# Optimization experiments

Hardware: AMD Instinct MI355X
Metric: run time of the kernel (lower is better)

Reference implementation:

```python
import jax, jax.numpy as jnp
import numpy as np

A_BITS = 4          # a_bits
W_BITS = 4          # w_bits / w_slices (w_slices = 1)
NUM_CHUNKS = 9      # ceil(in_ch*9 / 64) = ceil(576/64)
BN_EPS = 1e-5


def quantize_weight(w, bits):
    # WeightQuantize STE: uniform symmetric quantization, straight-through on clipped range
    n = 2.0 ** (bits - 1) - 1.0
    c = jnp.clip(w, -1.0, 1.0)
    q = jnp.round(c * n) / n
    return c + jax.lax.stop_gradient(q - c)


def create_input_stream(a, a_bits):
    # residual multi-bit binarization into a_bits sign planes, x ~= sum_i plane_i / 2^(i+1)
    x = jnp.clip(a, -1.0, 1.0)
    planes = []
    r = x
    for i in range(a_bits):
        s = jnp.where(r >= 0, 1.0, -1.0)
        planes.append(x + jax.lax.stop_gradient(s - x))  # STE plane
        r = r - s / (2.0 ** (i + 1))
    return jnp.stack(planes, 0)  # [a_bits, B, C*9, L]


def unfold3x3(x, pad=1):
    # torch F.unfold(kernel=3, stride=1) ordering: (C, kh, kw) flattened channel-major
    B, C, H, W = x.shape
    xp = jnp.pad(x, ((0, 0), (0, 0), (pad, pad), (pad, pad)))
    cols = jnp.stack([xp[:, :, i:i + H, j:j + W] for i in range(3) for j in range(3)], axis=2)
    return cols.reshape(B, C * 9, H * W)  # [B, C*9, L]


def mtj(x, gamma, beta, key):
    mean = x.mean(axis=(0, 2), keepdims=True)
    var = x.var(axis=(0, 2), keepdims=True)  # biased, as torch BN
    normed = (x - mean) / jnp.sqrt(var + BN_EPS) * gamma[None, :, None] + beta[None, :, None]
    t = jnp.tanh(4.0 * normed)
    rand = jax.random.uniform(key, x.shape, minval=-1.0, maxval=1.0)
    out = jnp.where(t > rand, 1.0, -1.0)
    out = jnp.where(normed == 0.0, 0.0, out)
    c = jnp.clip(normed, -1.0, 1.0)
    return c + jax.lax.stop_gradient(out - c)


def setup_inputs() -> dict:
    key = jax.random.key(0)
    k1, k2 = jax.random.split(key)
    inputs = jax.random.normal(k1, (8, 64, 32, 32), dtype=jnp.float32)
    weight = jax.random.normal(k2, (128, 64, 3, 3), dtype=jnp.float32) * (2.0 / (64 * 9)) ** 0.5
    gamma = jnp.ones((128,), jnp.float32)
    beta = jnp.zeros((128,), jnp.float32)
    return {"inputs": inputs, "weight": weight, "gamma": gamma, "beta": beta}


def reference(inputs, weight, gamma, beta):
    O = weight.shape[0]
    # weight standardization (per output filter; std is unbiased as torch .std())
    wf = weight.reshape(O, -1)
    bw = weight - wf.mean(-1)[:, None, None, None]
    std = bw.reshape(O, -1).std(-1, ddof=1)
    bw = bw / std[:, None, None, None]
    qw = quantize_weight(bw, W_BITS)                      # [O, C, 3, 3]
    a = unfold3x3(inputs)                                 # [B, C*9, L]
    stream = create_input_stream(a, A_BITS)               # [A, B, C*9, L]
    A, B, CK, L = stream.shape
    cs = CK // NUM_CHUNKS
    x = stream.reshape(A * B, NUM_CHUNKS, cs, L)          # chunked along the C*9 axis
    fw = qw.reshape(O, NUM_CHUNKS, cs)                    # flattened weight chunks
    # per-chunk F.linear, vectorized over chunks: [nc, A*B, O, L]
    lt = jnp.einsum('ngkl,ogk->gnol', x, fw)
    keys = jax.random.split(jax.random.key(42), NUM_CHUNKS)
    pre = jax.vmap(lambda t, k: mtj(t, gamma, beta, k))(lt, keys) / NUM_CHUNKS
    out = pre.sum(0)                                      # sum chunks (w_slices=1 -> identity combine)
    # gen_image_vector_and_sum: recombine activation bit-planes
    out = out.reshape(A, B, O, L)
    wts = (2.0 ** -(jnp.arange(A, dtype=jnp.float32) + 1.0)).reshape(A, 1, 1, 1)
    out = (out * wts).sum(0)
    HW = int(np.sqrt(L))
    return out.reshape(B, O, HW, HW)                      # F.fold with (1,1) kernel
```

## Files before the change

### kernel.cpp

```cpp
#include <hip/hip_runtime.h>
#include <stdint.h>

#ifndef PRNG_PARTITIONABLE
#define PRNG_PARTITIONABLE 1
#endif

#define ONE_M_U 0.99999994039535522461f

__device__ __forceinline__ void tf_4a(uint32_t& x0, uint32_t& x1){
  x0 += x1; x1 = (x1<<13)|(x1>>19); x1 ^= x0;
  x0 += x1; x1 = (x1<<15)|(x1>>17); x1 ^= x0;
  x0 += x1; x1 = (x1<<26)|(x1>>6);  x1 ^= x0;
  x0 += x1; x1 = (x1<<6) |(x1>>26); x1 ^= x0;
}
__device__ __forceinline__ void tf_4b(uint32_t& x0, uint32_t& x1){
  x0 += x1; x1 = (x1<<17)|(x1>>15); x1 ^= x0;
  x0 += x1; x1 = (x1<<29)|(x1>>3);  x1 ^= x0;
  x0 += x1; x1 = (x1<<16)|(x1>>16); x1 ^= x0;
  x0 += x1; x1 = (x1<<24)|(x1>>8);  x1 ^= x0;
}
__device__ __forceinline__ void threefry2x32(uint32_t k0, uint32_t k1, uint32_t& x0, uint32_t& x1){
  uint32_t k2 = k0 ^ k1 ^ 0x1BD11BDAu;
  x0 += k0; x1 += k1;
  tf_4a(x0,x1); x0 += k1; x1 += k2 + 1u;
  tf_4b(x0,x1); x0 += k2; x1 += k0 + 2u;
  tf_4a(x0,x1); x0 += k0; x1 += k1 + 3u;
  tf_4b(x0,x1); x0 += k1; x1 += k2 + 4u;
  tf_4a(x0,x1); x0 += k2; x1 += k0 + 5u;
}

__device__ __forceinline__ float bits_to_unit(uint32_t b){
  #pragma clang fp contract(off)
  float f = __uint_as_float((b >> 9) | 0x3f800000u) - 1.0f;
  float r = f * 2.0f + (-1.0f);
  return __builtin_fmaxf(-1.0f, r);
}

__device__ __forceinline__ float xla_tanh_f32(float x){
  #pragma clang fp contract(off)
  float ax = __builtin_fabsf(x);
  float xc = __builtin_fminf(__builtin_fmaxf(x, -9.0f), 9.0f);
  float x2 = xc * xc;
  float nm = -2.76076847742355e-16f;
  nm = x2 * nm + 2.00018790482477e-13f;
  nm = x2 * nm + -8.60467152213735e-11f;
  nm = x2 * nm + 5.12229709037114e-08f;
  nm = x2 * nm + 1.48572235717979e-05f;
  nm = x2 * nm + 6.37261928875436e-04f;
  nm = x2 * nm + 4.89352455891786e-03f;
  nm = xc * nm;
  float dn = 1.19825839466702e-06f;
  dn = x2 * dn + 1.18534705686654e-04f;
  dn = x2 * dn + 2.26843463243900e-03f;
  dn = x2 * dn + 4.89352518554385e-03f;
  float res = nm / dn;
  return (ax < 0.0004f) ? x : res;
}

__device__ __forceinline__ float dot64(unsigned long long sw, unsigned long long dw,
                                       const float* w){
  float acc = 0.0f;
  #pragma unroll
  for (int k = 0; k < 64; ++k){
    float mag = ((dw >> k) & 1ull) ? ONE_M_U : 1.0f;
    float p   = ((sw >> k) & 1ull) ? mag : -mag;
    acc = __builtin_fmaf(p, w[k], acc);
  }
  return acc;
}

#define QW_OFF   0u
#define QWT_OFF  294912u
#define SGN_OFF  589824u
#define DIM_OFF  2949120u
#define KEYS_OFF 5308416u
#define MV_OFF   5308544u
#define LT_OFF   5318656u
#define LT_BYTES 150994944u
#define WS_NEEDED_FAST (LT_OFF + LT_BYTES)

__global__ __launch_bounds__(64) void k_weights(const float* __restrict__ W,
        float* __restrict__ qw, float* __restrict__ qwT, uint32_t* __restrict__ keys){
  #pragma clang fp contract(off)
  __shared__ float  bwL[576];
  __shared__ double red[64];
  int o = blockIdx.x, t = threadIdx.x;
  double s = 0.0;
  for (int j = t; j < 576; j += 64) s += (double)W[o*576 + j];
  red[t] = s; __syncthreads();
  for (int k = 32; k > 0; k >>= 1){ if (t < k) red[t] += red[t+k]; __syncthreads(); }
  float mean1 = (float)(red[0] / 576.0);
  __syncthreads();
  for (int j = t; j < 576; j += 64) bwL[j] = W[o*576 + j] - mean1;
  __syncthreads();
  s = 0.0;
  for (int j = t; j < 576; j += 64) s += (double)bwL[j];
  red[t] = s; __syncthreads();
  for (int k = 32; k > 0; k >>= 1){ if (t < k) red[t] += red[t+k]; __syncthreads(); }
  float mean2 = (float)(red[0] / 576.0);
  __syncthreads();
  s = 0.0;
  for (int j = t; j < 576; j += 64){ float c = bwL[j] - mean2; float sq = c * c; s += (double)sq; }
  red[t] = s; __syncthreads();
  for (int k = 32; k > 0; k >>= 1){ if (t < k) red[t] += red[t+k]; __syncthreads(); }
  float varf = (float)(red[0] / 575.0);
  float stdv = __builtin_sqrtf(varf);
  __syncthreads();
  for (int j = t; j < 576; j += 64){
    float b2 = bwL[j] / stdv;
    float c  = __builtin_fminf(__builtin_fmaxf(b2, -1.0f), 1.0f);
    float q  = __builtin_rintf(c * 7.0f) / 7.0f;
    float fwd = c + (q - c);
    int g = j >> 6, k = j & 63;
    qw [(g*128 + o)*64 + k] = fwd;
    qwT[(g*64  + k)*128 + o] = fwd;
  }
  if (o == 0 && t == 0){
#if PRNG_PARTITIONABLE
    for (int g = 0; g < 9; ++g){
      uint32_t x0 = 0u, x1 = (uint32_t)g;
      threefry2x32(0u, 42u, x0, x1);
      keys[2*g] = x0; keys[2*g+1] = x1;
    }
#else
    uint32_t outv[18];
    for (int i = 0; i < 9; ++i){
      uint32_t x0 = (uint32_t)i, x1 = (uint32_t)(9 + i);
      threefry2x32(0u, 42u, x0, x1);
      outv[i] = x0; outv[9+i] = x1;
    }
    for (int j = 0; j < 18; ++j) keys[j] = outv[j];
#endif
  }
}

__global__ __launch_bounds__(256) void k_stream(const float* __restrict__ X,
        unsigned long long* __restrict__ sgn, unsigned long long* __restrict__ dimw){
  #pragma clang fp contract(off)
  int g = blockIdx.y;
  int tid = blockIdx.x * 256 + threadIdx.x;
  int b = tid >> 10, l = tid & 1023;
  int h = l >> 5, w = l & 31;
  unsigned long long sw0=0ull, sw1=0ull, sw2=0ull, sw3=0ull;
  unsigned long long dw0=0ull, dw1=0ull, dw2=0ull, dw3=0ull;
  const float* Xb = X + b*64*1024;
  int ck0 = g*64;
  #pragma unroll
  for (int i = 0; i < 64; ++i){
    int ck = ck0 + i;
    int c = ck / 9, kp = ck % 9;
    int di = kp / 3 - 1, dj = kp % 3 - 1;
    int hh = h + di, ww = w + dj;
    float v = 0.0f;
    if (hh >= 0 && hh < 32 && ww >= 0 && ww < 32)
      v = Xb[(c*32 + hh)*32 + ww];
    float x = __builtin_fminf(__builtin_fmaxf(v, -1.0f), 1.0f);
    float r = x;
    {
      float sv = (r >= 0.0f) ? 1.0f : -1.0f;
      float d  = sv - x;
      float p  = x + d;
      if (sv > 0.0f) sw0 |= (1ull << i);
      if (__builtin_fabsf(p) < 1.0f) dw0 |= (1ull << i);
      r = r - sv * 0.5f;
    }
    {
      float sv = (r >= 0.0f) ? 1.0f : -1.0f;
      float d  = sv - x;
      float p  = x + d;
      if (sv > 0.0f) sw1 |= (1ull << i);
      if (__builtin_fabsf(p) < 1.0f) dw1 |= (1ull << i);
      r = r - sv * 0.25f;
    }
    {
      float sv = (r >= 0.0f) ? 1.0f : -1.0f;
      float d  = sv - x;
      float p  = x + d;
      if (sv > 0.0f) sw2 |= (1ull << i);
      if (__builtin_fabsf(p) < 1.0f) dw2 |= (1ull << i);
      r = r - sv * 0.125f;
    }
    {
      float sv = (r >= 0.0f) ? 1.0f : -1.0f;
      float d  = sv - x;
      float p  = x + d;
      if (sv > 0.0f) sw3 |= (1ull << i);
      if (__builtin_fabsf(p) < 1.0f) dw3 |= (1ull << i);
      r = r - sv * 0.0625f;
    }
  }
  sgn [((0*8+b)*9 + g)*1024 + l] = sw0;
  sgn [((1*8+b)*9 + g)*1024 + l] = sw1;
  sgn [((2*8+b)*9 + g)*1024 + l] = sw2;
  sgn [((3*8+b)*9 + g)*1024 + l] = sw3;
  dimw[((0*8+b)*9 + g)*1024 + l] = dw0;
  dimw[((1*8+b)*9 + g)*1024 + l] = dw1;
  dimw[((2*8+b)*9 + g)*1024 + l] = dw2;
  dimw[((3*8+b)*9 + g)*1024 + l] = dw3;
}

__global__ __launch_bounds__(256) void k_gemm(const float* __restrict__ qwT,
        const unsigned long long* __restrict__ sgn, const unsigned long long* __restrict__ dimw,
        float* __restrict__ lt){
  __shared__ float wT[64*128];
  __shared__ float pL[64*64];
  int lchunk = blockIdx.x, g = blockIdx.y, n = blockIdx.z;
  int t = threadIdx.x;
  for (int j = t; j < 8192; j += 256) wT[j] = qwT[g*8192 + j];
  {
    int lc = t & 63, kq = t >> 6;
    unsigned long long sw = sgn [(n*9+g)*1024 + lchunk*64 + lc];
    unsigned long long dw = dimw[(n*9+g)*1024 + lchunk*64 + lc];
    #pragma unroll
    for (int kk = 0; kk < 16; ++kk){
      int k = kq*16 + kk;
      float mag = ((dw >> k) & 1ull) ? ONE_M_U : 1.0f;
      float p   = ((sw >> k) & 1ull) ? mag : -mag;
      pL[k*64 + lc] = p;
    }
  }
  __syncthreads();
  int otile = t & 31, ltile = t >> 5;
  const float4* wT4 = (const float4*)wT;
  const float4* pL4 = (const float4*)pL;
  float acc[4][8];
  #pragma unroll
  for (int i = 0; i < 4; ++i)
    #pragma unroll
    for (int j = 0; j < 8; ++j) acc[i][j] = 0.0f;
  #pragma unroll 8
  for (int k = 0; k < 64; ++k){
    float4 wv = wT4[k*32 + otile];
    float4 pa = pL4[k*16 + ltile*2];
    float4 pb = pL4[k*16 + ltile*2 + 1];
    float wr[4] = {wv.x, wv.y, wv.z, wv.w};
    float pr[8] = {pa.x, pa.y, pa.z, pa.w, pb.x, pb.y, pb.z, pb.w};
    #pragma unroll
    for (int i = 0; i < 4; ++i)
      #pragma unroll
      for (int j = 0; j < 8; ++j)
        acc[i][j] = __builtin_fmaf(pr[j], wr[i], acc[i][j]);
  }
  int o0 = otile*4, l0 = lchunk*64 + ltile*8;
  #pragma unroll
  for (int i = 0; i < 4; ++i){
    float* dst = lt + (((n*9+g)*128 + o0 + i) * 1024) + l0;
    float4 s0 = {acc[i][0], acc[i][1], acc[i][2], acc[i][3]};
    float4 s1 = {acc[i][4], acc[i][5], acc[i][6], acc[i][7]};
    ((float4*)dst)[0] = s0;
    ((float4*)dst)[1] = s1;
  }
}

__global__ __launch_bounds__(256) void k_stats_fast(const float* __restrict__ lt,
        float* __restrict__ mv){
  #pragma clang fp contract(off)
  __shared__ double red[256];
  int g = blockIdx.x >> 7, o = blockIdx.x & 127, t = threadIdx.x;
  double s1 = 0.0;
  for (int n = 0; n < 32; ++n){
    const float* p = lt + ((size_t)((n*9+g)*128 + o)) * 1024;
    for (int j = 0; j < 4; ++j) s1 += (double)p[t + j*256];
  }
  red[t] = s1; __syncthreads();
  for (int k = 128; k > 0; k >>= 1){ if (t < k) red[t] += red[t+k]; __syncthreads(); }
  float mean = (float)(red[0] / 32768.0);
  __syncthreads();
  double s2 = 0.0;
  for (int n = 0; n < 32; ++n){
    const float* p = lt + ((size_t)((n*9+g)*128 + o)) * 1024;
    for (int j = 0; j < 4; ++j){
      float tv = p[t + j*256];
      float c = tv - mean;
      float sq = c * c;
      s2 += (double)sq;
    }
  }
  red[t] = s2; __syncthreads();
  for (int k = 128; k > 0; k >>= 1){ if (t < k) red[t] += red[t+k]; __syncthreads(); }
  if (t == 0){
    float var = (float)(red[0] / 32768.0);
    float den = __builtin_sqrtf(var + 1e-5f);
    mv[(g*128+o)*2]   = mean;
    mv[(g*128+o)*2+1] = den;
  }
}

__global__ __launch_bounds__(256) void k_out_fast(const float* __restrict__ lt,
        const float* __restrict__ mv, const uint32_t* __restrict__ keys,
        const float* __restrict__ gamma, const float* __restrict__ beta,
        float* __restrict__ out){
  #pragma clang fp contract(off)
  __shared__ float    mvL[18];
  __shared__ uint32_t kL[18];
  int bi = blockIdx.x;
  int lc = bi & 3, o = (bi >> 2) & 127, b = bi >> 9;
  int t = threadIdx.x;
  if (t < 18){ mvL[t] = mv[((t>>1)*128 + o)*2 + (t&1)]; kL[t] = keys[t]; }
  __syncthreads();
  int l = lc*256 + t;
  float gma = gamma[o], bta = beta[o];
  float S[4] = {0.0f, 0.0f, 0.0f, 0.0f};
  for (int g = 0; g < 9; ++g){
    float rnd[4];
#if PRNG_PARTITIONABLE
    #pragma unroll
    for (int a = 0; a < 4; ++a){
      uint32_t m = (uint32_t)((a*8 + b)*131072 + o*1024 + l);
      uint32_t x0 = 0u, x1 = m;
      threefry2x32(kL[2*g], kL[2*g+1], x0, x1);
      rnd[a] = bits_to_unit(x0 ^ x1);
    }
#else
    #pragma unroll
    for (int a01 = 0; a01 < 2; ++a01){
      uint32_t m = (uint32_t)((a01*8 + b)*131072 + o*1024 + l);
      uint32_t x0 = m, x1 = m + 2097152u;
      threefry2x32(kL[2*g], kL[2*g+1], x0, x1);
      rnd[a01]     = bits_to_unit(x0);
      rnd[a01 + 2] = bits_to_unit(x1);
    }
#endif
    float mean = mvL[2*g], den = mvL[2*g+1];
    #pragma unroll
    for (int a = 0; a < 4; ++a){
      int n = a*8 + b;
      float tv = lt[((size_t)((n*9+g)*128 + o)) * 1024 + l];
      float normed = (tv - mean) / den * gma + bta;
      float th = xla_tanh_f32(4.0f * normed);
      float dec = (th > rnd[a]) ? 1.0f : -1.0f;
      if (normed == 0.0f) dec = 0.0f;
      float cc  = __builtin_fminf(__builtin_fmaxf(normed, -1.0f), 1.0f);
      float fwd = cc + (dec - cc);
      float pre = fwd / 9.0f;
      S[a] = S[a] + pre;
    }
  }
  float z = S[0] * 0.5f;
  z = z + S[1] * 0.25f;
  z = z + S[2] * 0.125f;
  z = z + S[3] * 0.0625f;
  out[(b*128 + o)*1024 + l] = z;
}

__global__ __launch_bounds__(256) void k_stats_slow(const float* __restrict__ qw,
        const unsigned long long* __restrict__ sgn, const unsigned long long* __restrict__ dimw,
        float* __restrict__ mv){
  #pragma clang fp contract(off)
  __shared__ double red[256];
  int g = blockIdx.x >> 7, o = blockIdx.x & 127, t = threadIdx.x;
  float wr[64];
  #pragma unroll
  for (int k = 0; k < 64; ++k) wr[k] = qw[(g*128 + o)*64 + k];
  double s1 = 0.0;
  for (int n = 0; n < 32; ++n){
    const unsigned long long* sp = sgn  + (n*9 + g)*1024;
    const unsigned long long* dp = dimw + (n*9 + g)*1024;
    for (int j = 0; j < 4; ++j){
      int l = t + j*256;
      float tv = dot64(sp[l], dp[l], wr);
      s1 += (double)tv;
    }
  }
  red[t] = s1; __syncthreads();
  for (int k = 128; k > 0; k >>= 1){ if (t < k) red[t] += red[t+k]; __syncthreads(); }
  float mean = (float)(red[0] / 32768.0);
  __syncthreads();
  double s2 = 0.0;
  for (int n = 0; n < 32; ++n){
    const unsigned long long* sp = sgn  + (n*9 + g)*1024;
    const unsigned long long* dp = dimw + (n*9 + g)*1024;
    for (int j = 0; j < 4; ++j){
      int l = t + j*256;
      float tv = dot64(sp[l], dp[l], wr);
      float c = tv - mean;
      float sq = c * c;
      s2 += (double)sq;
    }
  }
  red[t] = s2; __syncthreads();
  for (int k = 128; k > 0; k >>= 1){ if (t < k) red[t] += red[t+k]; __syncthreads(); }
  if (t == 0){
    float var = (float)(red[0] / 32768.0);
    float den = __builtin_sqrtf(var + 1e-5f);
    mv[(g*128+o)*2]   = mean;
    mv[(g*128+o)*2+1] = den;
  }
}

__global__ __launch_bounds__(256) void k_out_slow(const float* __restrict__ qw,
        const unsigned long long* __restrict__ sgn, const unsigned long long* __restrict__ dimw,
        const float* __restrict__ mv, const uint32_t* __restrict__ keys,
        const float* __restrict__ gamma, const float* __restrict__ beta,
        float* __restrict__ out){
  #pragma clang fp contract(off)
  __shared__ float    wv[576];
  __shared__ float    mvL[18];
  __shared__ uint32_t kL[18];
  int bi = blockIdx.x;
  int lc = bi & 3, o = (bi >> 2) & 127, b = bi >> 9;
  int t = threadIdx.x;
  for (int j = t; j < 576; j += 256) wv[j] = qw[((j >> 6)*128 + o)*64 + (j & 63)];
  if (t < 18){ mvL[t] = mv[((t>>1)*128 + o)*2 + (t&1)]; kL[t] = keys[t]; }
  __syncthreads();
  int l = lc*256 + t;
  float gma = gamma[o], bta = beta[o];
  float S[4] = {0.0f, 0.0f, 0.0f, 0.0f};
  for (int g = 0; g < 9; ++g){
    float rnd[4];
#if PRNG_PARTITIONABLE
    #pragma unroll
    for (int a = 0; a < 4; ++a){
      uint32_t m = (uint32_t)((a*8 + b)*131072 + o*1024 + l);
      uint32_t x0 = 0u, x1 = m;
      threefry2x32(kL[2*g], kL[2*g+1], x0, x1);
      rnd[a] = bits_to_unit(x0 ^ x1);
    }
#else
    #pragma unroll
    for (int a01 = 0; a01 < 2; ++a01){
      uint32_t m = (uint32_t)((a01*8 + b)*131072 + o*1024 + l);
      uint32_t x0 = m, x1 = m + 2097152u;
      threefry2x32(kL[2*g], kL[2*g+1], x0, x1);
      rnd[a01]     = bits_to_unit(x0);
      rnd[a01 + 2] = bits_to_unit(x1);
    }
#endif
    float mean = mvL[2*g], den = mvL[2*g+1];
    float wr[64];
    #pragma unroll
    for (int k = 0; k < 64; ++k) wr[k] = wv[g*64 + k];
    #pragma unroll
    for (int a = 0; a < 4; ++a){
      int n = a*8 + b;
      float tv = dot64(sgn[(n*9+g)*1024 + l], dimw[(n*9+g)*1024 + l], wr);
      float normed = (tv - mean) / den * gma + bta;
      float th = xla_tanh_f32(4.0f * normed);
      float dec = (th > rnd[a]) ? 1.0f : -1.0f;
      if (normed == 0.0f) dec = 0.0f;
      float cc  = __builtin_fminf(__builtin_fmaxf(normed, -1.0f), 1.0f);
      float fwd = cc + (dec - cc);
      float pre = fwd / 9.0f;
      S[a] = S[a] + pre;
    }
  }
  float z = S[0] * 0.5f;
  z = z + S[1] * 0.25f;
  z = z + S[2] * 0.125f;
  z = z + S[3] * 0.0625f;
  out[(b*128 + o)*1024 + l] = z;
}

extern "C" void kernel_launch(void* const* d_in, const int* in_sizes, int n_in,
                              void* d_out, int out_size, void* d_ws, size_t ws_size,
                              hipStream_t stream){
  (void)in_sizes; (void)n_in; (void)out_size;
  const float* inp   = (const float*)d_in[0];
  const float* wgt   = (const float*)d_in[1];
  const float* gamma = (const float*)d_in[2];
  const float* beta  = (const float*)d_in[3];
  float* out = (float*)d_out;
  char* ws = (char*)d_ws;
  float*              qw   = (float*)(ws + QW_OFF);
  float*              qwT  = (float*)(ws + QWT_OFF);
  unsigned long long* sgn  = (unsigned long long*)(ws + SGN_OFF);
  unsigned long long* dimw = (unsigned long long*)(ws + DIM_OFF);
  uint32_t*           keys = (uint32_t*)(ws + KEYS_OFF);
  float*              mv   = (float*)(ws + MV_OFF);
  float*              lt   = (float*)(ws + LT_OFF);

  hipLaunchKernelGGL(k_weights, dim3(128),    dim3(64),  0, stream, wgt, qw, qwT, keys);
  hipLaunchKernelGGL(k_stream,  dim3(32, 9),  dim3(256), 0, stream, inp, sgn, dimw);
  if (ws_size >= (size_t)WS_NEEDED_FAST){
    hipLaunchKernelGGL(k_gemm,       dim3(16, 9, 32), dim3(256), 0, stream, qwT, sgn, dimw, lt);
    hipLaunchKernelGGL(k_stats_fast, dim3(1152),      dim3(256), 0, stream, lt, mv);
    hipLaunchKernelGGL(k_out_fast,   dim3(4096),      dim3(256), 0, stream, lt, mv, keys,
                       gamma, beta, out);
  } else {
    hipLaunchKernelGGL(k_stats_slow, dim3(1152), dim3(256), 0, stream, qw, sgn, dimw, mv);
    hipLaunchKernelGGL(k_out_slow,   dim3(4096), dim3(256), 0, stream, qw, sgn, dimw, mv, keys,
                       gamma, beta, out);
  }
}
```

Measured before the change: 331.3 us.

## Fuse per-channel mean partials into GEMM epilogue and retile GEMM to 128x128

The GEMM now computes a 128x128 output tile per block from padded LDS float4 tiles taken straight from qw, which removes the transposed weight copy. Its epilogue reduces per-channel partial sums in double precision and writes them to a new partial buffer. A small k_mean kernel turns those partials into the channel mean, so the stats kernel only makes one pass over lt for the variance. The output kernel loop order is swapped so each bit-plane walks the chunks with a single base pointer. This spends one extra launch and more workspace to avoid re-reading the 150MB lt buffer for the mean.

After: 322.2 us. -2.7%, faster.

```diff
diff --git a/kernel.cpp b/kernel.cpp
--- a/kernel.cpp
+++ b/kernel.cpp
@@ -70,17 +70,18 @@
 }
 
 #define QW_OFF   0u
-#define QWT_OFF  294912u
-#define SGN_OFF  589824u
-#define DIM_OFF  2949120u
-#define KEYS_OFF 5308416u
-#define MV_OFF   5308544u
-#define LT_OFF   5318656u
+#define SGN_OFF  294912u
+#define DIM_OFF  2654208u
+#define KEYS_OFF 5013504u
+#define MV_OFF   5013632u
+#define LT_OFF   5023744u
 #define LT_BYTES 150994944u
-#define WS_NEEDED_FAST (LT_OFF + LT_BYTES)
+#define PART_OFF (LT_OFF + LT_BYTES)
+#define PART_BYTES 2359296u
+#define WS_NEEDED_FAST (PART_OFF + PART_BYTES)
 
 __global__ __launch_bounds__(64) void k_weights(const float* __restrict__ W,
-        float* __restrict__ qw, float* __restrict__ qwT, uint32_t* __restrict__ keys){
+        float* __restrict__ qw, uint32_t* __restrict__ keys){
   #pragma clang fp contract(off)
   __shared__ float  bwL[576];
   __shared__ double red[64];
@@ -113,7 +114,6 @@
     float fwd = c + (q - c);
     int g = j >> 6, k = j & 63;
     qw [(g*128 + o)*64 + k] = fwd;
-    qwT[(g*64  + k)*128 + o] = fwd;
   }
   if (o == 0 && t == 0){
 #if PRNG_PARTITIONABLE
@@ -158,32 +158,28 @@
     float r = x;
     {
       float sv = (r >= 0.0f) ? 1.0f : -1.0f;
-      float d  = sv - x;
-      float p  = x + d;
+      float d  = sv - x; float p = x + d;
       if (sv > 0.0f) sw0 |= (1ull << i);
       if (__builtin_fabsf(p) < 1.0f) dw0 |= (1ull << i);
       r = r - sv * 0.5f;
     }
     {
       float sv = (r >= 0.0f) ? 1.0f : -1.0f;
-      float d  = sv - x;
-      float p  = x + d;
+      float d  = sv - x; float p = x + d;
       if (sv > 0.0f) sw1 |= (1ull << i);
       if (__builtin_fabsf(p) < 1.0f) dw1 |= (1ull << i);
       r = r - sv * 0.25f;
     }
     {
       float sv = (r >= 0.0f) ? 1.0f : -1.0f;
-      float d  = sv - x;
-      float p  = x + d;
+      float d  = sv - x; float p = x + d;
       if (sv > 0.0f) sw2 |= (1ull << i);
       if (__builtin_fabsf(p) < 1.0f) dw2 |= (1ull << i);
       r = r - sv * 0.125f;
     }
     {
       float sv = (r >= 0.0f) ? 1.0f : -1.0f;
-      float d  = sv - x;
-      float p  = x + d;
+      float d  = sv - x; float p = x + d;
       if (sv > 0.0f) sw3 |= (1ull << i);
       if (__builtin_fabsf(p) < 1.0f) dw3 |= (1ull << i);
       r = r - sv * 0.0625f;
@@ -199,73 +195,106 @@
   dimw[((3*8+b)*9 + g)*1024 + l] = dw3;
 }
 
-__global__ __launch_bounds__(256) void k_gemm(const float* __restrict__ qwT,
+__global__ __launch_bounds__(256) void k_gemm(const float* __restrict__ qw,
         const unsigned long long* __restrict__ sgn, const unsigned long long* __restrict__ dimw,
-        float* __restrict__ lt){
-  __shared__ float wT[64*128];
-  __shared__ float pL[64*64];
-  int lchunk = blockIdx.x, g = blockIdx.y, n = blockIdx.z;
+        float* __restrict__ lt, double* __restrict__ part){
+  __shared__ float4 wS[128*17];
+  __shared__ float4 pS[128*17];
+  int lq = blockIdx.x, g = blockIdx.y, n = blockIdx.z;
   int t = threadIdx.x;
-  for (int j = t; j < 8192; j += 256) wT[j] = qwT[g*8192 + j];
   {
-    int lc = t & 63, kq = t >> 6;
-    unsigned long long sw = sgn [(n*9+g)*1024 + lchunk*64 + lc];
-    unsigned long long dw = dimw[(n*9+g)*1024 + lchunk*64 + lc];
-    #pragma unroll
-    for (int kk = 0; kk < 16; ++kk){
-      int k = kq*16 + kk;
-      float mag = ((dw >> k) & 1ull) ? ONE_M_U : 1.0f;
-      float p   = ((sw >> k) & 1ull) ? mag : -mag;
-      pL[k*64 + lc] = p;
-    }
-  }
-  __syncthreads();
-  int otile = t & 31, ltile = t >> 5;
-  const float4* wT4 = (const float4*)wT;
-  const float4* pL4 = (const float4*)pL;
-  float acc[4][8];
-  #pragma unroll
-  for (int i = 0; i < 4; ++i)
+    int o = t >> 4, kq = t & 15;
+    const float4* qw4 = (const float4*)qw;
+    #pragma unroll
+    for (int i = 0; i < 8; ++i){
+      int oo = o + 16*i;
+      wS[oo*17 + kq] = qw4[(g*128 + oo)*16 + kq];
+    }
+  }
+  {
+    int l = t >> 1, kh = t & 1;
+    unsigned long long sw = sgn [(n*9+g)*1024 + lq*128 + l];
+    unsigned long long dw = dimw[(n*9+g)*1024 + lq*128 + l];
+    #pragma unroll
+    for (int kq = 0; kq < 8; ++kq){
+      int kqq = kh*8 + kq;
+      float4 v;
+      {
+        int k = kqq*4;
+        float m0 = ((dw>>k)&1ull)?ONE_M_U:1.0f; v.x = ((sw>>k)&1ull)?m0:-m0;
+        float m1 = ((dw>>(k+1))&1ull)?ONE_M_U:1.0f; v.y = ((sw>>(k+1))&1ull)?m1:-m1;
+        float m2 = ((dw>>(k+2))&1ull)?ONE_M_U:1.0f; v.z = ((sw>>(k+2))&1ull)?m2:-m2;
+        float m3 = ((dw>>(k+3))&1ull)?ONE_M_U:1.0f; v.w = ((sw>>(k+3))&1ull)?m3:-m3;
+      }
+      pS[l*17 + kqq] = v;
+    }
+  }
+  __syncthreads();
+  int ot = t >> 4, ltl = t & 15;
+  float acc[8][8];
+  #pragma unroll
+  for (int i = 0; i < 8; ++i)
     #pragma unroll
     for (int j = 0; j < 8; ++j) acc[i][j] = 0.0f;
-  #pragma unroll 8
-  for (int k = 0; k < 64; ++k){
-    float4 wv = wT4[k*32 + otile];
-    float4 pa = pL4[k*16 + ltile*2];
-    float4 pb = pL4[k*16 + ltile*2 + 1];
-    float wr[4] = {wv.x, wv.y, wv.z, wv.w};
-    float pr[8] = {pa.x, pa.y, pa.z, pa.w, pb.x, pb.y, pb.z, pb.w};
-    #pragma unroll
-    for (int i = 0; i < 4; ++i)
+  for (int kq = 0; kq < 16; ++kq){
+    float wr[8][4], pr[8][4];
+    #pragma unroll
+    for (int i = 0; i < 8; ++i) *(float4*)wr[i] = wS[(ot*8+i)*17 + kq];
+    #pragma unroll
+    for (int j = 0; j < 8; ++j) *(float4*)pr[j] = pS[(ltl+16*j)*17 + kq];
+    #pragma unroll
+    for (int e = 0; e < 4; ++e)
       #pragma unroll
-      for (int j = 0; j < 8; ++j)
-        acc[i][j] = __builtin_fmaf(pr[j], wr[i], acc[i][j]);
-  }
-  int o0 = otile*4, l0 = lchunk*64 + ltile*8;
-  #pragma unroll
-  for (int i = 0; i < 4; ++i){
-    float* dst = lt + (((n*9+g)*128 + o0 + i) * 1024) + l0;
-    float4 s0 = {acc[i][0], acc[i][1], acc[i][2], acc[i][3]};
-    float4 s1 = {acc[i][4], acc[i][5], acc[i][6], acc[i][7]};
-    ((float4*)dst)[0] = s0;
-    ((float4*)dst)[1] = s1;
-  }
-}
-
-__global__ __launch_bounds__(256) void k_stats_fast(const float* __restrict__ lt,
+      for (int i = 0; i < 8; ++i)
+        #pragma unroll
+        for (int j = 0; j < 8; ++j)
+          acc[i][j] = __builtin_fmaf(pr[j][e], wr[i][e], acc[i][j]);
+  }
+  #pragma unroll
+  for (int i = 0; i < 8; ++i){
+    int o = ot*8 + i;
+    float* dst = lt + ((size_t)((n*9+g)*128 + o))*1024 + lq*128 + ltl;
+    #pragma unroll
+    for (int j = 0; j < 8; ++j) dst[16*j] = acc[i][j];
+  }
+  double ps[8];
+  #pragma unroll
+  for (int i = 0; i < 8; ++i){
+    double s = 0.0;
+    #pragma unroll
+    for (int j = 0; j < 8; ++j) s += (double)acc[i][j];
+    ps[i] = s;
+  }
+  __syncthreads();
+  double* red = (double*)pS;
+  #pragma unroll
+  for (int i = 0; i < 8; ++i) red[(ot*8+i)*16 + ltl] = ps[i];
+  __syncthreads();
+  if (t < 128){
+    double s = 0.0;
+    #pragma unroll
+    for (int q = 0; q < 16; ++q) s += red[t*16 + q];
+    part[((size_t)g*128 + t)*256 + n*8 + lq] = s;
+  }
+}
+
+__global__ __launch_bounds__(64) void k_mean(const double* __restrict__ part,
+        float* __restrict__ mv){
+  __shared__ double red[64];
+  int go = blockIdx.x, t = threadIdx.x;
+  double s = 0.0;
+  for (int idx = t; idx < 256; idx += 64) s += part[(size_t)go*256 + idx];
+  red[t] = s; __syncthreads();
+  for (int k = 32; k > 0; k >>= 1){ if (t < k) red[t] += red[t+k]; __syncthreads(); }
+  if (t == 0) mv[go*2] = (float)(red[0] / 32768.0);
+}
+
+__global__ __launch_bounds__(256) void k_stats2(const float* __restrict__ lt,
         float* __restrict__ mv){
   #pragma clang fp contract(off)
   __shared__ double red[256];
   int g = blockIdx.x >> 7, o = blockIdx.x & 127, t = threadIdx.x;
-  double s1 = 0.0;
-  for (int n = 0; n < 32; ++n){
-    const float* p = lt + ((size_t)((n*9+g)*128 + o)) * 1024;
-    for (int j = 0; j < 4; ++j) s1 += (double)p[t + j*256];
-  }
-  red[t] = s1; __syncthreads();
-  for (int k = 128; k > 0; k >>= 1){ if (t < k) red[t] += red[t+k]; __syncthreads(); }
-  float mean = (float)(red[0] / 32768.0);
-  __syncthreads();
+  float mean = mv[(g*128+o)*2];
   double s2 = 0.0;
   for (int n = 0; n < 32; ++n){
     const float* p = lt + ((size_t)((n*9+g)*128 + o)) * 1024;
@@ -281,7 +310,6 @@
   if (t == 0){
     float var = (float)(red[0] / 32768.0);
     float den = __builtin_sqrtf(var + 1e-5f);
-    mv[(g*128+o)*2]   = mean;
     mv[(g*128+o)*2+1] = den;
   }
 }
@@ -300,41 +328,39 @@
   __syncthreads();
   int l = lc*256 + t;
   float gma = gamma[o], bta = beta[o];
-  float S[4] = {0.0f, 0.0f, 0.0f, 0.0f};
-  for (int g = 0; g < 9; ++g){
-    float rnd[4];
+  float S[4];
+  #pragma unroll
+  for (int a = 0; a < 4; ++a){
+    int n = a*8 + b;
 #if PRNG_PARTITIONABLE
-    #pragma unroll
-    for (int a = 0; a < 4; ++a){
-      uint32_t m = (uint32_t)((a*8 + b)*131072 + o*1024 + l);
+    uint32_t m = (uint32_t)(n*131072 + o*1024 + l);
+#endif
+    const float* pa = lt + ((size_t)(n*9)*128 + o)*1024 + l;
+    float Sa = 0.0f;
+    for (int g = 0; g < 9; ++g){
+      float rnd;
+#if PRNG_PARTITIONABLE
       uint32_t x0 = 0u, x1 = m;
       threefry2x32(kL[2*g], kL[2*g+1], x0, x1);
-      rnd[a] = bits_to_unit(x0 ^ x1);
-    }
+      rnd = bits_to_unit(x0 ^ x1);
 #else
-    #pragma unroll
-    for (int a01 = 0; a01 < 2; ++a01){
-      uint32_t m = (uint32_t)((a01*8 + b)*131072 + o*1024 + l);
-      uint32_t x0 = m, x1 = m + 2097152u;
+      uint32_t mm = (uint32_t)(((a&1)*8 + b)*131072 + o*1024 + l);
+      uint32_t x0 = mm, x1 = mm + 2097152u;
       threefry2x32(kL[2*g], kL[2*g+1], x0, x1);
-      rnd[a01]     = bits_to_unit(x0);
-      rnd[a01 + 2] = bits_to_unit(x1);
-    }
+      rnd = (a < 2) ? bits_to_unit(x0) : bits_to_unit(x1);
 #endif
-    float mean = mvL[2*g], den = mvL[2*g+1];
-    #pragma unroll
-    for (int a = 0; a < 4; ++a){
-      int n = a*8 + b;
-      float tv = lt[((size_t)((n*9+g)*128 + o)) * 1024 + l];
+      float mean = mvL[2*g], den = mvL[2*g+1];
+      float tv = pa[g*131072];
       float normed = (tv - mean) / den * gma + bta;
       float th = xla_tanh_f32(4.0f * normed);
-      float dec = (th > rnd[a]) ? 1.0f : -1.0f;
+      float dec = (th > rnd) ? 1.0f : -1.0f;
       if (normed == 0.0f) dec = 0.0f;
       float cc  = __builtin_fminf(__builtin_fmaxf(normed, -1.0f), 1.0f);
       float fwd = cc + (dec - cc);
       float pre = fwd / 9.0f;
-      S[a] = S[a] + pre;
-    }
+      Sa = Sa + pre;
+    }
+    S[a] = Sa;
   }
   float z = S[0] * 0.5f;
   z = z + S[1] * 0.25f;
@@ -462,19 +488,20 @@
   float* out = (float*)d_out;
   char* ws = (char*)d_ws;
   float*              qw   = (float*)(ws + QW_OFF);
-  float*              qwT  = (float*)(ws + QWT_OFF);
   unsigned long long* sgn  = (unsigned long long*)(ws + SGN_OFF);
   unsigned long long* dimw = (unsigned long long*)(ws + DIM_OFF);
   uint32_t*           keys = (uint32_t*)(ws + KEYS_OFF);
   float*              mv   = (float*)(ws + MV_OFF);
   float*              lt   = (float*)(ws + LT_OFF);
-
-  hipLaunchKernelGGL(k_weights, dim3(128),    dim3(64),  0, stream, wgt, qw, qwT, keys);
+  double*             part = (double*)(ws + PART_OFF);
+
+  hipLaunchKernelGGL(k_weights, dim3(128),    dim3(64),  0, stream, wgt, qw, keys);
   hipLaunchKernelGGL(k_stream,  dim3(32, 9),  dim3(256), 0, stream, inp, sgn, dimw);
   if (ws_size >= (size_t)WS_NEEDED_FAST){
-    hipLaunchKernelGGL(k_gemm,       dim3(16, 9, 32), dim3(256), 0, stream, qwT, sgn, dimw, lt);
-    hipLaunchKernelGGL(k_stats_fast, dim3(1152),      dim3(256), 0, stream, lt, mv);
-    hipLaunchKernelGGL(k_out_fast,   dim3(4096),      dim3(256), 0, stream, lt, mv, keys,
+    hipLaunchKernelGGL(k_gemm,   dim3(8, 9, 32), dim3(256), 0, stream, qw, sgn, dimw, lt, part);
+    hipLaunchKernelGGL(k_mean,   dim3(1152),     dim3(64),  0, stream, part, mv);
+    hipLaunchKernelGGL(k_stats2, dim3(1152),     dim3(256), 0, stream, lt, mv);
+    hipLaunchKernelGGL(k_out_fast, dim3(4096),   dim3(256), 0, stream, lt, mv, keys,
                        gamma, beta, out);
   } else {
     hipLaunchKernelGGL(k_stats_slow, dim3(1152), dim3(256), 0, stream, qw, sgn, dimw, mv);
```
